# Kernel tuning notes

Measured on AMD Instinct MI355X. Metric: run time of the kernel, lower is better.

The kernel has to match this reference:

```python
import jax, jax.numpy as jnp
import numpy as np

N = 8192        # num_drugs
D_EMB = 256     # args.gcn_hidden3 (global encoder input)
D_FEAT = 256    # args.hidden_size (local encoder input)
H1 = H2 = H3 = 256  # args.ff_hidden1/2/3
LOG2 = float(np.log(2.0))
ADJ_DENSITY = 0.01


def _ff(x, w1, b1, w2, b2, w3, b3, ws, bs):
    # FF block: 3-layer ReLU MLP + linear shortcut (FF_local / FF_global)
    h = jax.nn.relu(x @ w1 + b1)
    h = jax.nn.relu(h @ w2 + b2)
    h = jax.nn.relu(h @ w3 + b3)
    return h + x @ ws + bs


def _lin_init(k, fan_in, fan_out):
    s = 1.0 / np.sqrt(fan_in)
    kw, kb = jax.random.split(k)
    w = jax.random.uniform(kw, (fan_in, fan_out), minval=-s, maxval=s, dtype=jnp.float32)
    b = jax.random.uniform(kb, (fan_out,), minval=-s, maxval=s, dtype=jnp.float32)
    return w, b


def setup_inputs() -> dict:
    key = jax.random.key(0)
    ks = jax.random.split(key, 11)
    g_w1, g_b1 = _lin_init(ks[0], D_EMB, H1)
    g_w2, g_b2 = _lin_init(ks[1], H1, H2)
    g_w3, g_b3 = _lin_init(ks[2], H2, H3)
    g_ws, g_bs = _lin_init(ks[3], D_EMB, H3)
    l_w1, l_b1 = _lin_init(ks[4], D_FEAT, H1)
    l_w2, l_b2 = _lin_init(ks[5], H1, H2)
    l_w3, l_b3 = _lin_init(ks[6], H2, H3)
    l_ws, l_bs = _lin_init(ks[7], D_FEAT, H3)
    embeddings = jax.random.normal(ks[8], (N, D_EMB), dtype=jnp.float32)
    features = jax.random.normal(ks[9], (N, D_FEAT), dtype=jnp.float32)
    adj_tensor = (jax.random.uniform(ks[10], (N, N)) < ADJ_DENSITY).astype(jnp.float32)
    return dict(embeddings=embeddings, features=features, adj_tensor=adj_tensor,
                num_drugs=N,
                g_w1=g_w1, g_b1=g_b1, g_w2=g_w2, g_b2=g_b2, g_w3=g_w3, g_b3=g_b3,
                g_ws=g_ws, g_bs=g_bs,
                l_w1=l_w1, l_b1=l_b1, l_w2=l_w2, l_b2=l_b2, l_w3=l_w3, l_b3=l_b3,
                l_ws=l_ws, l_bs=l_bs)


def reference(embeddings, features, adj_tensor,
              g_w1, g_b1, g_w2, g_b2, g_w3, g_b3, g_ws, g_bs,
              l_w1, l_b1, l_w2, l_b2, l_w3, l_b3, l_ws, l_bs,
              num_drugs):
    g_enc = _ff(embeddings, g_w1, g_b1, g_w2, g_b2, g_w3, g_b3, g_ws, g_bs)  # [N, H3]
    l_enc = _ff(features,   l_w1, l_b1, l_w2, l_b2, l_w3, l_b3, l_ws, l_bs)  # [N, H3]
    res = l_enc @ g_enc.T                      # [N, N] pairwise local-global scores
    pos_mask = adj_tensor
    neg_mask = 1.0 - adj_tensor
    # JSD estimator (as in InfoGraph/MIRACLE: mask applied BEFORE the expectation)
    p = res * pos_mask
    E_pos = jnp.sum(LOG2 - jax.nn.softplus(-p)) / num_drugs
    q = res * neg_mask
    E_neg = jnp.sum(jax.nn.softplus(-q) + q - LOG2) / (num_drugs * (num_drugs - 1))
    return E_neg - E_pos  # prior=False -> PRIOR term is 0
```

## Files before the change

### kernel.cpp

```cpp
#include <hip/hip_runtime.h>
#include <hip/hip_bf16.h>
#include <stdint.h>

typedef __bf16 bf16;
typedef __bf16 bf16x8 __attribute__((ext_vector_type(8)));
typedef float f32x4 __attribute__((ext_vector_type(4)));

#define N_DRUGS 8192
#define DIM 256
#define LOG2_C 0.6931471805599453f
#define W_POS (1.0f / 8192.0f)
#define W_NEG (1.0f / (8192.0f * 8191.0f))

__device__ inline void gload_lds16(const void* g, void* l) {
  __builtin_amdgcn_global_load_lds(
      (const __attribute__((address_space(1))) void*)g,
      (__attribute__((address_space(3))) void*)l, 16, 0, 0);
}

__device__ inline int swz(int row, int c) {
  return (c & ~7) | ((c ^ row) & 7);
}

__device__ inline float load_as_f32(const void* p, size_t idx, int dt_bf16) {
  return dt_bf16 ? (float)((const bf16*)p)[idx] : ((const float*)p)[idx];
}

__global__ void detect_dtype(const unsigned short* emb, int* flag) {
  int l = threadIdx.x & 63;
  unsigned short u = emb[2 * l];
  int e = (u >> 7) & 0xFF;
  int plausible = (e >= 96 && e <= 140) || (u == 0);
  unsigned long long m = __ballot(plausible);
  if (l == 0) *flag = (__popcll(m) >= 32) ? 1 : 0;
}

struct P8 { const void* p[8]; };

__global__ __launch_bounds__(256) void transpose_w(P8 srcs, bf16* wt,
                                                   const int* flag) {
  __shared__ bf16 t[32][33];
  const int dt = *flag;
  int m = blockIdx.z;
  const void* src = srcs.p[m];
  bf16* dst = wt + m * 65536;
  int bx = blockIdx.x * 32;
  int by = blockIdx.y * 32;
  int tx = threadIdx.x, ty = threadIdx.y;
#pragma unroll
  for (int i = 0; i < 32; i += 8)
    t[ty + i][tx] = (bf16)load_as_f32(src, (size_t)(by + ty + i) * DIM + bx + tx, dt);
  __syncthreads();
#pragma unroll
  for (int i = 0; i < 32; i += 8)
    dst[(bx + ty + i) * DIM + by + tx] = t[tx][ty + i];
}

struct FFArgs {
  const void *x, *b1, *b2, *b3, *bs;
  const bf16 *wt1, *wt2, *wt3, *wts;
  bf16* out;
};
struct FFBoth { FFArgs a[2]; };

__global__ __launch_bounds__(256) void ff_kernel(FFBoth both, const int* flag) {
  __shared__ __align__(16) bf16 xin[64 * 256];
  __shared__ __align__(16) bf16 cur[64 * 256];
  const FFArgs A = (blockIdx.y == 0) ? both.a[0] : both.a[1];
  const int dt = *flag;

  const int t = threadIdx.x;
  const int w = t >> 6, l = t & 63;
  const int lm = l & 15, lq = l >> 4;
  const int n0 = w * 64;
  const int r0 = blockIdx.x * 64;

  if (dt) {
#pragma unroll
    for (int it = 0; it < 8; ++it) {
      int ci = it * 256 + t, row = ci >> 5, c = ci & 31;
      *(bf16x8*)&xin[row * 256 + swz(row, c) * 8] =
          *(const bf16x8*)&((const bf16*)A.x)[(size_t)(r0 + row) * DIM + c * 8];
    }
  } else {
#pragma unroll
    for (int it = 0; it < 8; ++it) {
      int ci = it * 256 + t, row = ci >> 5, c = ci & 31;
      const float* src = &((const float*)A.x)[(size_t)(r0 + row) * DIM + c * 8];
      bf16x8 v;
#pragma unroll
      for (int e = 0; e < 8; ++e) v[e] = (bf16)src[e];
      *(bf16x8*)&xin[row * 256 + swz(row, c) * 8] = v;
    }
  }
  __syncthreads();

  f32x4 acc[4][4];
  const f32x4 fz = {0.f, 0.f, 0.f, 0.f};

  auto compute = [&](const bf16* src, const bf16* wt) {
#pragma unroll
    for (int i = 0; i < 4; ++i)
#pragma unroll
      for (int j = 0; j < 4; ++j) acc[i][j] = fz;
#pragma unroll
    for (int ks = 0; ks < 256; ks += 32) {
      bf16x8 af[4], bfr[4];
#pragma unroll
      for (int i = 0; i < 4; ++i) {
        int row = i * 16 + lm;
        int k = ks + lq * 8;
        af[i] = *(const bf16x8*)&src[row * 256 + swz(row, k >> 3) * 8];
      }
#pragma unroll
      for (int j = 0; j < 4; ++j) {
        int n = n0 + j * 16 + lm;
        bfr[j] = *(const bf16x8*)&wt[n * DIM + ks + lq * 8];
      }
#pragma unroll
      for (int i = 0; i < 4; ++i)
#pragma unroll
        for (int j = 0; j < 4; ++j)
          acc[i][j] = __builtin_amdgcn_mfma_f32_16x16x32_bf16(af[i], bfr[j],
                                                              acc[i][j], 0, 0, 0);
    }
  };

  auto store_relu = [&](const void* bias) {
    __syncthreads();
#pragma unroll
    for (int j = 0; j < 4; ++j) {
      int col = n0 + j * 16 + lm;
      float bj = load_as_f32(bias, col, dt);
      int cc = col >> 3, cw = col & 7;
#pragma unroll
      for (int i = 0; i < 4; ++i)
#pragma unroll
        for (int r = 0; r < 4; ++r) {
          int row = i * 16 + lq * 4 + r;
          float v = fmaxf(acc[i][j][r] + bj, 0.f);
          cur[row * 256 + swz(row, cc) * 8 + cw] = (bf16)v;
        }
    }
    __syncthreads();
  };

  compute(xin, A.wt1); store_relu(A.b1);
  compute(cur, A.wt2); store_relu(A.b2);
  compute(cur, A.wt3); store_relu(A.b3);
  compute(xin, A.wts);

#pragma unroll
  for (int j = 0; j < 4; ++j) {
    int col = n0 + j * 16 + lm;
    float bj = load_as_f32(A.bs, col, dt);
    int cc = col >> 3, cw = col & 7;
#pragma unroll
    for (int i = 0; i < 4; ++i)
#pragma unroll
      for (int r = 0; r < 4; ++r) {
        int row = i * 16 + lq * 4 + r;
        float h3 = (float)cur[row * 256 + swz(row, cc) * 8 + cw];
        float v = acc[i][j][r] + bj + h3;
        A.out[(size_t)(r0 + row) * DIM + col] = (bf16)v;
      }
  }
}

__global__ __launch_bounds__(256) void gemm_reduce(const bf16* __restrict__ Lenc,
                                                   const bf16* __restrict__ Genc,
                                                   const void* __restrict__ adj,
                                                   float* accum, const int* flag) {
  __shared__ __align__(16) bf16 At[128 * 64];
  __shared__ __align__(16) bf16 Bt[128 * 64];
  __shared__ float red[256];

  const int dt = *flag;
  const int t = threadIdx.x;
  const int w = t >> 6, l = t & 63;
  const int wr = w >> 1, wc = w & 1;
  const int lm = l & 15, lq = l >> 4;
  const int row0 = blockIdx.y * 128;
  const int col0 = blockIdx.x * 128;

  f32x4 acc[4][4];
  const f32x4 fz = {0.f, 0.f, 0.f, 0.f};
#pragma unroll
  for (int i = 0; i < 4; ++i)
#pragma unroll
    for (int j = 0; j < 4; ++j) acc[i][j] = fz;

  for (int kk = 0; kk < 256; kk += 64) {
    __syncthreads();
#pragma unroll
    for (int it = 0; it < 4; ++it) {
      int ci = it * 256 + t;
      int row = ci >> 3, cs = ci & 7;
      int cg = swz(row, cs);
      bf16* lbase = &At[(it * 256 + w * 64) * 8];
      gload_lds16(&Lenc[(size_t)(row0 + row) * DIM + kk + cg * 8], lbase);
      bf16* lbase2 = &Bt[(it * 256 + w * 64) * 8];
      gload_lds16(&Genc[(size_t)(col0 + row) * DIM + kk + cg * 8], lbase2);
    }
    __syncthreads();
#pragma unroll
    for (int ks = 0; ks < 64; ks += 32) {
      bf16x8 af[4], bfr[4];
#pragma unroll
      for (int i = 0; i < 4; ++i) {
        int row = wr * 64 + i * 16 + lm;
        int kc = (ks >> 3) + lq;
        af[i] = *(const bf16x8*)&At[row * 64 + swz(row, kc) * 8];
      }
#pragma unroll
      for (int j = 0; j < 4; ++j) {
        int row = wc * 64 + j * 16 + lm;
        int kc = (ks >> 3) + lq;
        bfr[j] = *(const bf16x8*)&Bt[row * 64 + swz(row, kc) * 8];
      }
#pragma unroll
      for (int i = 0; i < 4; ++i)
#pragma unroll
        for (int j = 0; j < 4; ++j)
          acc[i][j] = __builtin_amdgcn_mfma_f32_16x16x32_bf16(af[i], bfr[j],
                                                              acc[i][j], 0, 0, 0);
    }
  }

  float lsum = 0.f;
#pragma unroll
  for (int i = 0; i < 4; ++i) {
#pragma unroll
    for (int r = 0; r < 4; ++r) {
      int rr = row0 + wr * 64 + i * 16 + lq * 4 + r;
      size_t abase = (size_t)rr * N_DRUGS + col0 + wc * 64;
#pragma unroll
      for (int j = 0; j < 4; ++j) {
        float res = acc[i][j][r];
        float a = load_as_f32(adj, abase + j * 16 + lm, dt);
        float s = fmaxf(res, 0.f) + __logf(1.f + __expf(-fabsf(res)));
        float vneg = (s - LOG2_C) * W_NEG;
        float vpos = (s - res - LOG2_C) * W_POS;
        lsum += (a > 0.5f) ? vpos : vneg;
      }
    }
  }

  red[t] = lsum;
  __syncthreads();
#pragma unroll
  for (int sft = 128; sft > 0; sft >>= 1) {
    if (t < sft) red[t] += red[t + sft];
    __syncthreads();
  }
  if (t == 0) atomicAdd(accum, red[0]);
}

__global__ void finalize_k(const float* accum, unsigned int* out) {
  if (threadIdx.x == 0 && blockIdx.x == 0) {
    float v = *accum;
    union { bf16 h; unsigned short u; } cv;
    cv.h = (bf16)v;
    out[0] = ((unsigned int)cv.u << 16) | cv.u;
  }
}

extern "C" void kernel_launch(void* const* d_in, const int* in_sizes, int n_in,
                              void* d_out, int out_size, void* d_ws, size_t ws_size,
                              hipStream_t stream) {
  const void* embeddings = d_in[0];
  const void* features   = d_in[1];
  const void* adj        = d_in[2];

  char* ws = (char*)d_ws;
  float* accum = (float*)ws;
  int* flag = (int*)(ws + 64);
  bf16* wt   = (bf16*)(ws + 1024);
  bf16* genc = (bf16*)(ws + 1024 + 8 * 65536 * 2);
  bf16* lenc = (bf16*)(ws + 1024 + 8 * 65536 * 2 + (size_t)N_DRUGS * DIM * 2);

  hipMemsetAsync(accum, 0, sizeof(float), stream);

  detect_dtype<<<1, 64, 0, stream>>>((const unsigned short*)embeddings, flag);

  P8 srcs;
  srcs.p[0] = d_in[4];  srcs.p[1] = d_in[6];  srcs.p[2] = d_in[8];  srcs.p[3] = d_in[10];
  srcs.p[4] = d_in[12]; srcs.p[5] = d_in[14]; srcs.p[6] = d_in[16]; srcs.p[7] = d_in[18];
  transpose_w<<<dim3(8, 8, 8), dim3(32, 8), 0, stream>>>(srcs, wt, flag);

  FFBoth fb;
  fb.a[0] = FFArgs{embeddings, d_in[5], d_in[7], d_in[9], d_in[11],
                   wt + 0 * 65536, wt + 1 * 65536, wt + 2 * 65536, wt + 3 * 65536,
                   genc};
  fb.a[1] = FFArgs{features, d_in[13], d_in[15], d_in[17], d_in[19],
                   wt + 4 * 65536, wt + 5 * 65536, wt + 6 * 65536, wt + 7 * 65536,
                   lenc};
  ff_kernel<<<dim3(128, 2), 256, 0, stream>>>(fb, flag);

  gemm_reduce<<<dim3(64, 64), 256, 0, stream>>>(lenc, genc, adj, accum, flag);

  finalize_k<<<1, 64, 0, stream>>>(accum, (unsigned int*)d_out);
}
```

Baseline: 460.2 us.

## Fold dtype detection and finalize into kernels, prefetch adjacency, widen FF blocks

Removes the separate dtype-detect and finalize launches: each kernel sniffs the input dtype itself, and the last GEMM block, found through an atomic counter, writes the output. The adjacency values for each thread are loaded into registers before the GEMM main loop so their latency overlaps the MFMA work. The block reduction now uses wave shuffles instead of a shared-memory tree. The FF kernel moves to 512 threads with 8 waves each covering 32 columns. The GEMM also gets a launch-bounds occupancy hint. Holding 64 adjacency registers per thread raises register pressure and may limit occupancy.

Measured after the change: 527.4 us. 14.6% more time.

```diff
diff --git a/kernel.cpp b/kernel.cpp
--- a/kernel.cpp
+++ b/kernel.cpp
@@ -26,21 +26,22 @@
   return dt_bf16 ? (float)((const bf16*)p)[idx] : ((const float*)p)[idx];
 }
 
-__global__ void detect_dtype(const unsigned short* emb, int* flag) {
+__device__ inline int sniff_dt(const void* x) {
+  const unsigned short* u16p = (const unsigned short*)x;
   int l = threadIdx.x & 63;
-  unsigned short u = emb[2 * l];
+  unsigned short u = u16p[2 * l];
   int e = (u >> 7) & 0xFF;
   int plausible = (e >= 96 && e <= 140) || (u == 0);
   unsigned long long m = __ballot(plausible);
-  if (l == 0) *flag = (__popcll(m) >= 32) ? 1 : 0;
+  return (__popcll(m) >= 32) ? 1 : 0;
 }
 
 struct P8 { const void* p[8]; };
 
 __global__ __launch_bounds__(256) void transpose_w(P8 srcs, bf16* wt,
-                                                   const int* flag) {
+                                                   const void* emb) {
   __shared__ bf16 t[32][33];
-  const int dt = *flag;
+  const int dt = sniff_dt(emb);
   int m = blockIdx.z;
   const void* src = srcs.p[m];
   bf16* dst = wt + m * 65536;
@@ -63,29 +64,29 @@
 };
 struct FFBoth { FFArgs a[2]; };
 
-__global__ __launch_bounds__(256) void ff_kernel(FFBoth both, const int* flag) {
+__global__ __launch_bounds__(512) void ff_kernel(FFBoth both) {
   __shared__ __align__(16) bf16 xin[64 * 256];
   __shared__ __align__(16) bf16 cur[64 * 256];
   const FFArgs A = (blockIdx.y == 0) ? both.a[0] : both.a[1];
-  const int dt = *flag;
+  const int dt = sniff_dt(A.x);
 
   const int t = threadIdx.x;
   const int w = t >> 6, l = t & 63;
   const int lm = l & 15, lq = l >> 4;
-  const int n0 = w * 64;
+  const int n0 = w * 32;
   const int r0 = blockIdx.x * 64;
 
   if (dt) {
 #pragma unroll
-    for (int it = 0; it < 8; ++it) {
-      int ci = it * 256 + t, row = ci >> 5, c = ci & 31;
+    for (int it = 0; it < 4; ++it) {
+      int ci = it * 512 + t, row = ci >> 5, c = ci & 31;
       *(bf16x8*)&xin[row * 256 + swz(row, c) * 8] =
           *(const bf16x8*)&((const bf16*)A.x)[(size_t)(r0 + row) * DIM + c * 8];
     }
   } else {
 #pragma unroll
-    for (int it = 0; it < 8; ++it) {
-      int ci = it * 256 + t, row = ci >> 5, c = ci & 31;
+    for (int it = 0; it < 4; ++it) {
+      int ci = it * 512 + t, row = ci >> 5, c = ci & 31;
       const float* src = &((const float*)A.x)[(size_t)(r0 + row) * DIM + c * 8];
       bf16x8 v;
 #pragma unroll
@@ -95,32 +96,31 @@
   }
   __syncthreads();
 
-  f32x4 acc[4][4];
+  f32x4 acc[4][2];
   const f32x4 fz = {0.f, 0.f, 0.f, 0.f};
 
   auto compute = [&](const bf16* src, const bf16* wt) {
 #pragma unroll
     for (int i = 0; i < 4; ++i)
 #pragma unroll
-      for (int j = 0; j < 4; ++j) acc[i][j] = fz;
+      for (int j = 0; j < 2; ++j) acc[i][j] = fz;
 #pragma unroll
     for (int ks = 0; ks < 256; ks += 32) {
-      bf16x8 af[4], bfr[4];
+      bf16x8 af[4], bfr[2];
 #pragma unroll
       for (int i = 0; i < 4; ++i) {
         int row = i * 16 + lm;
-        int k = ks + lq * 8;
-        af[i] = *(const bf16x8*)&src[row * 256 + swz(row, k >> 3) * 8];
-      }
-#pragma unroll
-      for (int j = 0; j < 4; ++j) {
+        af[i] = *(const bf16x8*)&src[row * 256 + swz(row, (ks >> 3) + lq) * 8];
+      }
+#pragma unroll
+      for (int j = 0; j < 2; ++j) {
         int n = n0 + j * 16 + lm;
         bfr[j] = *(const bf16x8*)&wt[n * DIM + ks + lq * 8];
       }
 #pragma unroll
       for (int i = 0; i < 4; ++i)
 #pragma unroll
-        for (int j = 0; j < 4; ++j)
+        for (int j = 0; j < 2; ++j)
           acc[i][j] = __builtin_amdgcn_mfma_f32_16x16x32_bf16(af[i], bfr[j],
                                                               acc[i][j], 0, 0, 0);
     }
@@ -129,7 +129,7 @@
   auto store_relu = [&](const void* bias) {
     __syncthreads();
 #pragma unroll
-    for (int j = 0; j < 4; ++j) {
+    for (int j = 0; j < 2; ++j) {
       int col = n0 + j * 16 + lm;
       float bj = load_as_f32(bias, col, dt);
       int cc = col >> 3, cw = col & 7;
@@ -151,7 +151,7 @@
   compute(xin, A.wts);
 
 #pragma unroll
-  for (int j = 0; j < 4; ++j) {
+  for (int j = 0; j < 2; ++j) {
     int col = n0 + j * 16 + lm;
     float bj = load_as_f32(A.bs, col, dt);
     int cc = col >> 3, cw = col & 7;
@@ -167,21 +167,46 @@
   }
 }
 
-__global__ __launch_bounds__(256) void gemm_reduce(const bf16* __restrict__ Lenc,
-                                                   const bf16* __restrict__ Genc,
-                                                   const void* __restrict__ adj,
-                                                   float* accum, const int* flag) {
+__global__ __launch_bounds__(256, 2) void gemm_reduce(
+    const bf16* __restrict__ Lenc, const bf16* __restrict__ Genc,
+    const void* __restrict__ adj, const void* __restrict__ emb,
+    float* accum, unsigned* counter, unsigned* out) {
   __shared__ __align__(16) bf16 At[128 * 64];
   __shared__ __align__(16) bf16 Bt[128 * 64];
-  __shared__ float red[256];
-
-  const int dt = *flag;
+  __shared__ float red[4];
+
+  const int dt = sniff_dt(emb);
   const int t = threadIdx.x;
   const int w = t >> 6, l = t & 63;
   const int wr = w >> 1, wc = w & 1;
   const int lm = l & 15, lq = l >> 4;
   const int row0 = blockIdx.y * 128;
   const int col0 = blockIdx.x * 128;
+
+  unsigned apu[64];
+  const int rbase = row0 + wr * 64 + lq * 4;
+  const int cbase = col0 + wc * 64 + lm;
+  if (dt) {
+    const unsigned short* A_ = (const unsigned short*)adj;
+#pragma unroll
+    for (int i = 0; i < 4; ++i)
+#pragma unroll
+      for (int r = 0; r < 4; ++r)
+#pragma unroll
+        for (int j = 0; j < 4; ++j)
+          apu[(i * 4 + r) * 4 + j] =
+              A_[(size_t)(rbase + i * 16 + r) * N_DRUGS + cbase + j * 16];
+  } else {
+    const unsigned* A_ = (const unsigned*)adj;
+#pragma unroll
+    for (int i = 0; i < 4; ++i)
+#pragma unroll
+      for (int r = 0; r < 4; ++r)
+#pragma unroll
+        for (int j = 0; j < 4; ++j)
+          apu[(i * 4 + r) * 4 + j] =
+              A_[(size_t)(rbase + i * 16 + r) * N_DRUGS + cbase + j * 16];
+  }
 
   f32x4 acc[4][4];
   const f32x4 fz = {0.f, 0.f, 0.f, 0.f};
@@ -209,14 +234,12 @@
 #pragma unroll
       for (int i = 0; i < 4; ++i) {
         int row = wr * 64 + i * 16 + lm;
-        int kc = (ks >> 3) + lq;
-        af[i] = *(const bf16x8*)&At[row * 64 + swz(row, kc) * 8];
+        af[i] = *(const bf16x8*)&At[row * 64 + swz(row, (ks >> 3) + lq) * 8];
       }
 #pragma unroll
       for (int j = 0; j < 4; ++j) {
         int row = wc * 64 + j * 16 + lm;
-        int kc = (ks >> 3) + lq;
-        bfr[j] = *(const bf16x8*)&Bt[row * 64 + swz(row, kc) * 8];
+        bfr[j] = *(const bf16x8*)&Bt[row * 64 + swz(row, (ks >> 3) + lq) * 8];
       }
 #pragma unroll
       for (int i = 0; i < 4; ++i)
@@ -229,39 +252,33 @@
 
   float lsum = 0.f;
 #pragma unroll
-  for (int i = 0; i < 4; ++i) {
-#pragma unroll
-    for (int r = 0; r < 4; ++r) {
-      int rr = row0 + wr * 64 + i * 16 + lq * 4 + r;
-      size_t abase = (size_t)rr * N_DRUGS + col0 + wc * 64;
+  for (int i = 0; i < 4; ++i)
+#pragma unroll
+    for (int r = 0; r < 4; ++r)
 #pragma unroll
       for (int j = 0; j < 4; ++j) {
         float res = acc[i][j][r];
-        float a = load_as_f32(adj, abase + j * 16 + lm, dt);
         float s = fmaxf(res, 0.f) + __logf(1.f + __expf(-fabsf(res)));
         float vneg = (s - LOG2_C) * W_NEG;
         float vpos = (s - res - LOG2_C) * W_POS;
-        lsum += (a > 0.5f) ? vpos : vneg;
-      }
-    }
-  }
-
-  red[t] = lsum;
+        lsum += (apu[(i * 4 + r) * 4 + j] != 0u) ? vpos : vneg;
+      }
+
+#pragma unroll
+  for (int off = 32; off > 0; off >>= 1) lsum += __shfl_down(lsum, off, 64);
+  if (l == 0) red[w] = lsum;
   __syncthreads();
-#pragma unroll
-  for (int sft = 128; sft > 0; sft >>= 1) {
-    if (t < sft) red[t] += red[t + sft];
-    __syncthreads();
-  }
-  if (t == 0) atomicAdd(accum, red[0]);
-}
-
-__global__ void finalize_k(const float* accum, unsigned int* out) {
-  if (threadIdx.x == 0 && blockIdx.x == 0) {
-    float v = *accum;
-    union { bf16 h; unsigned short u; } cv;
-    cv.h = (bf16)v;
-    out[0] = ((unsigned int)cv.u << 16) | cv.u;
+  if (t == 0) {
+    atomicAdd(accum, red[0] + red[1] + red[2] + red[3]);
+    __threadfence();
+    unsigned old = atomicAdd(counter, 1u);
+    if (old == 64 * 64 - 1) {
+      __threadfence();
+      float v = atomicAdd(accum, 0.0f);
+      union { bf16 h; unsigned short u; } cv;
+      cv.h = (bf16)v;
+      out[0] = ((unsigned)cv.u << 16) | cv.u;
+    }
   }
 }
 
@@ -274,19 +291,17 @@
 
   char* ws = (char*)d_ws;
   float* accum = (float*)ws;
-  int* flag = (int*)(ws + 64);
+  unsigned* counter = (unsigned*)(ws + 4);
   bf16* wt   = (bf16*)(ws + 1024);
   bf16* genc = (bf16*)(ws + 1024 + 8 * 65536 * 2);
   bf16* lenc = (bf16*)(ws + 1024 + 8 * 65536 * 2 + (size_t)N_DRUGS * DIM * 2);
 
-  hipMemsetAsync(accum, 0, sizeof(float), stream);
-
-  detect_dtype<<<1, 64, 0, stream>>>((const unsigned short*)embeddings, flag);
+  hipMemsetAsync(ws, 0, 8, stream);
 
   P8 srcs;
   srcs.p[0] = d_in[4];  srcs.p[1] = d_in[6];  srcs.p[2] = d_in[8];  srcs.p[3] = d_in[10];
   srcs.p[4] = d_in[12]; srcs.p[5] = d_in[14]; srcs.p[6] = d_in[16]; srcs.p[7] = d_in[18];
-  transpose_w<<<dim3(8, 8, 8), dim3(32, 8), 0, stream>>>(srcs, wt, flag);
+  transpose_w<<<dim3(8, 8, 8), dim3(32, 8), 0, stream>>>(srcs, wt, embeddings);
 
   FFBoth fb;
   fb.a[0] = FFArgs{embeddings, d_in[5], d_in[7], d_in[9], d_in[11],
@@ -295,9 +310,8 @@
   fb.a[1] = FFArgs{features, d_in[13], d_in[15], d_in[17], d_in[19],
                    wt + 4 * 65536, wt + 5 * 65536, wt + 6 * 65536, wt + 7 * 65536,
                    lenc};
-  ff_kernel<<<dim3(128, 2), 256, 0, stream>>>(fb, flag);
-
-  gemm_reduce<<<dim3(64, 64), 256, 0, stream>>>(lenc, genc, adj, accum, flag);
-
-  finalize_k<<<1, 64, 0, stream>>>(accum, (unsigned int*)d_out);
-}
+  ff_kernel<<<dim3(128, 2), 512, 0, stream>>>(fb);
+
+  gemm_reduce<<<dim3(64, 64), 256, 0, stream>>>(lenc, genc, adj, embeddings,
+                                                accum, counter, (unsigned*)d_out);
+}
```
